# Performance work log

Hardware: AMD Instinct MI355X
Metric: run time of the kernel (lower is better)

Reference implementation:

```python
import jax, jax.numpy as jnp
import numpy as np

NUM_CODEBOOKS = 2
CODEBOOK_SIZE = 256
OUT_GROUP = 1
IN_GROUP = 8
IN_FEATURES = 4096
OUT_FEATURES = 11008


def setup_inputs() -> dict:
    key = jax.random.key(0)
    k1, k2, k3, k4, k5 = jax.random.split(key, 5)
    num_out_groups = OUT_FEATURES // OUT_GROUP
    num_in_groups = IN_FEATURES // IN_GROUP
    x = jax.random.normal(k1, (4, 2048, IN_FEATURES), dtype=jnp.float32)
    codes = jax.random.randint(k2, (num_out_groups, num_in_groups, NUM_CODEBOOKS), 0, CODEBOOK_SIZE, dtype=jnp.int32)
    codebooks = jax.random.normal(k3, (NUM_CODEBOOKS, CODEBOOK_SIZE, OUT_GROUP, IN_GROUP), dtype=jnp.float32) * 0.05
    scales = jax.random.uniform(k4, (num_out_groups, 1, 1, 1), dtype=jnp.float32)
    bias = jax.random.normal(k5, (OUT_FEATURES,), dtype=jnp.float32)
    return {"x": x, "codes": codes, "codebooks": codebooks, "scales": scales, "bias": bias}


def _dequantize_weight(codes, codebooks, scales):
    # codes: [Og, Ig, C] int; codebooks: [C, K, og, ig]; scales: [Og,1,1,1]
    C = codebooks.shape[0]
    og, ig = codebooks.shape[2], codebooks.shape[3]
    Og, Ig = codes.shape[0], codes.shape[1]
    # gather per-codebook vectors: result [Og, Ig, C, og, ig]
    w = codebooks[jnp.arange(C)[None, None, :], codes]
    w = w.sum(axis=2)                      # [Og, Ig, og, ig] (additive quantization)
    w = w * scales                         # broadcast [Og,1,1,1]
    w = w.transpose(0, 2, 1, 3)            # [Og, og, Ig, ig]
    return w.reshape(Og * og, Ig * ig)     # [out_features, in_features]


def reference(x, codes, codebooks, scales, bias):
    W = _dequantize_weight(codes, codebooks, scales)
    return jnp.einsum('bsi,oi->bso', x, W) + bias
```

## Files before the change

### kernel.cpp

```cpp
#include <hip/hip_runtime.h>
#include <hip/hip_bf16.h>
#include <stdint.h>

#define IN_F 4096
#define OUT_F 11008
#define M_ROWS 8192
#define NIG 512
#define CBSZ 256

typedef _Float16 f16x8 __attribute__((ext_vector_type(8)));
typedef float f32x4 __attribute__((ext_vector_type(4)));

__global__ __launch_bounds__(256) void dequant_w_kernel(
    const int* __restrict__ codes, const float* __restrict__ cbs,
    _Float16* __restrict__ W)
{
  const int idx = blockIdx.x * 256 + threadIdx.x;
  const int2 c = ((const int2*)codes)[idx];
  const float4* e0 = (const float4*)(cbs + (size_t)c.x * 8);
  const float4* e1 = (const float4*)(cbs + (size_t)CBSZ * 8 + (size_t)c.y * 8);
  const float4 a0 = e0[0], a1 = e0[1];
  const float4 b0 = e1[0], b1 = e1[1];
  f16x8 w;
  w[0] = (_Float16)(a0.x + b0.x);
  w[1] = (_Float16)(a0.y + b0.y);
  w[2] = (_Float16)(a0.z + b0.z);
  w[3] = (_Float16)(a0.w + b0.w);
  w[4] = (_Float16)(a1.x + b1.x);
  w[5] = (_Float16)(a1.y + b1.y);
  w[6] = (_Float16)(a1.z + b1.z);
  w[7] = (_Float16)(a1.w + b1.w);
  *(f16x8*)(W + (size_t)idx * 8) = w;
}

__global__ __launch_bounds__(256) void convert_x_kernel(
    const float* __restrict__ x, _Float16* __restrict__ X)
{
  const size_t i = ((size_t)blockIdx.x * 256 + threadIdx.x) * 8;
  const float4 a = *(const float4*)(x + i);
  const float4 b = *(const float4*)(x + i + 4);
  f16x8 v;
  v[0] = (_Float16)a.x; v[1] = (_Float16)a.y;
  v[2] = (_Float16)a.z; v[3] = (_Float16)a.w;
  v[4] = (_Float16)b.x; v[5] = (_Float16)b.y;
  v[6] = (_Float16)b.z; v[7] = (_Float16)b.w;
  *(f16x8*)(X + i) = v;
}

#define BM 256
#define BN 256
#define BK 64
#define NKT (IN_F / BK)
#define GRID_MT (M_ROWS / BM)
#define GRID_NT (OUT_F / BN)

__global__ __launch_bounds__(512, 2) void gemm_pipe(
    const _Float16* __restrict__ X, const _Float16* __restrict__ Wd,
    const float* __restrict__ scales, const float* __restrict__ bias,
    float* __restrict__ out)
{
  __shared__ char smem[131072];

  const int cpx = (GRID_MT * GRID_NT) >> 3;
  const int wg = (blockIdx.x & 7) * cpx + (blockIdx.x >> 3);
  const int mt = wg & (GRID_MT - 1), nt = wg >> 5;
  const int m0 = mt * BM, n0 = nt * BN;

  const int t_ = threadIdx.x;
  const int wave = t_ >> 6, lane = t_ & 63;
  const int wm = wave >> 2, wn = wave & 3;
  const int r16 = lane & 15;
  const int q = lane >> 4;
  const int sw = r16 & 7;
  const int c0 = ((q ^ sw) << 4);
  const int c1 = (((4 | q) ^ sw) << 4);

  const int s_row0 = t_ >> 3;
  const int s_col  = (((t_ & 7) ^ ((t_ >> 3) & 7)) << 3);
  const _Float16* asrc = X  + (size_t)(m0 + s_row0) * IN_F + s_col;
  const _Float16* bsrc = Wd + (size_t)(n0 + s_row0) * IN_F + s_col;
  const int s_dst = wave * 1024;

  f32x4 acc[8][4] = {};
  f16x8 al0[4], al1[4], ah0[4], ah1[4], bl0[2], bl1[2], bh0[2], bh1[2];

#define GLD(gsrc, ldst) __builtin_amdgcn_global_load_lds(                     \
    (const __attribute__((address_space(1))) void*)(gsrc),                    \
    (__attribute__((address_space(3))) void*)(ldst), 16, 0, 0)
#define STAGE_A(kt, bufc, i) GLD(asrc + (size_t)(kt) * BK + (size_t)(i) * 64 * IN_F, \
    smem + (bufc) * 65536 + (i) * 8192 + s_dst)
#define STAGE_B(kt, bufc, i) GLD(bsrc + (size_t)(kt) * BK + (size_t)(i) * 64 * IN_F, \
    smem + (bufc) * 65536 + 32768 + (i) * 8192 + s_dst)

#define RD_A(bufp, mm, cc) (*(const f16x8*)((bufp) + ((wm * 128 + (mm) * 16 + r16) << 7) + (cc)))
#define RD_B(bufp, nn, cc) (*(const f16x8*)((bufp) + 32768 + ((wn * 64 + (nn) * 16 + r16) << 7) + (cc)))

#define BAR   __builtin_amdgcn_s_barrier()
#define PRIO1 __builtin_amdgcn_s_setprio(1)
#define PRIO0 __builtin_amdgcn_s_setprio(0)
#define SBAR0 __builtin_amdgcn_sched_barrier(0)
#define VM0 asm volatile("s_waitcnt vmcnt(0)" ::: "memory")

#define MG(AF, BF, MO, NO)                                                    \
    _Pragma("unroll")                                                         \
    for (int m = 0; m < 4; ++m)                                               \
      _Pragma("unroll")                                                       \
      for (int n = 0; n < 2; ++n)                                             \
        acc[(MO) + m][(NO) + n] = __builtin_amdgcn_mfma_f32_16x16x32_f16(     \
            AF[m], BF[n], acc[(MO) + m][(NO) + n], 0, 0, 0)

#define TILE(P, tt, STG, GATE) do {                                           \
    const char* bufT = smem + (P) * 65536;                                    \
    if (STG) {                                                                \
      STAGE_A((tt) + 1, 1 - (P), 0); STAGE_A((tt) + 1, 1 - (P), 1);           \
      STAGE_A((tt) + 1, 1 - (P), 2); STAGE_A((tt) + 1, 1 - (P), 3);           \
      STAGE_B((tt) + 1, 1 - (P), 0); STAGE_B((tt) + 1, 1 - (P), 1);           \
      STAGE_B((tt) + 1, 1 - (P), 2); STAGE_B((tt) + 1, 1 - (P), 3);           \
    }                                                                         \
    SBAR0;                                                                    \
         \
    _Pragma("unroll")                                                         \
    for (int m = 0; m < 4; ++m) al0[m] = RD_A(bufT, m, c0);                   \
    _Pragma("unroll")                                                         \
    for (int n = 0; n < 2; ++n) { bl0[n] = RD_B(bufT, n, c0);                 \
                                  bh0[n] = RD_B(bufT, 2 + n, c0); }           \
    _Pragma("unroll")                                                         \
    for (int m = 0; m < 4; ++m) ah0[m] = RD_A(bufT, 4 + m, c0);               \
    SBAR0;                                                                    \
    PRIO1;                                                                    \
    MG(al0, bl0, 0, 0); MG(al0, bh0, 0, 2);                                   \
    MG(ah0, bh0, 4, 2); MG(ah0, bl0, 4, 0);                                   \
    PRIO0;                                                                    \
    SBAR0;                                                                    \
                                                           \
    _Pragma("unroll")                                                         \
    for (int m = 0; m < 4; ++m) al1[m] = RD_A(bufT, m, c1);                   \
    _Pragma("unroll")                                                         \
    for (int n = 0; n < 2; ++n) { bl1[n] = RD_B(bufT, n, c1);                 \
                                  bh1[n] = RD_B(bufT, 2 + n, c1); }           \
    _Pragma("unroll")                                                         \
    for (int m = 0; m < 4; ++m) ah1[m] = RD_A(bufT, 4 + m, c1);               \
    SBAR0;                                                                    \
    PRIO1;                                                                    \
    MG(al1, bl1, 0, 0); MG(al1, bh1, 0, 2);                                   \
    MG(ah1, bh1, 4, 2); MG(ah1, bl1, 4, 0);                                   \
    PRIO0;                                                                    \
    SBAR0;                                                                    \
    if (GATE) { VM0; BAR; }       \
  } while (0)

  STAGE_A(0, 0, 0); STAGE_A(0, 0, 1); STAGE_A(0, 0, 2); STAGE_A(0, 0, 3);
  STAGE_B(0, 0, 0); STAGE_B(0, 0, 1); STAGE_B(0, 0, 2); STAGE_B(0, 0, 3);
  VM0;
  BAR;

  #pragma unroll 1
  for (int t = 0; t < 62; t += 2) {
    TILE(0, t,     1, 1);
    TILE(1, t + 1, 1, 1);
  }
  TILE(0, 62, 1, 1);
  TILE(1, 63, 0, 0);

  const int crow = (lane >> 4) << 2;
  #pragma unroll
  for (int nf = 0; nf < 4; ++nf) {
    const int col = n0 + wn * 64 + nf * 16 + r16;
    const float s = scales[col];
    const float bb = bias[col];
    #pragma unroll
    for (int mf = 0; mf < 8; ++mf) {
      const int rb = m0 + wm * 128 + mf * 16 + crow;
      #pragma unroll
      for (int r = 0; r < 4; ++r)
        out[(size_t)(rb + r) * OUT_F + col] = acc[mf][nf][r] * s + bb;
    }
  }
#undef TILE
#undef MG
#undef RD_A
#undef RD_B
#undef STAGE_A
#undef STAGE_B
#undef GLD
}

__global__ __launch_bounds__(256) void naive_kernel(
    const float* __restrict__ x, const int* __restrict__ codes,
    const float* __restrict__ cbs, const float* __restrict__ scales,
    const float* __restrict__ bias, float* __restrict__ out)
{
  __shared__ float xrow[IN_F];
  const int m = blockIdx.x;
  for (int i = threadIdx.x; i < IN_F; i += 256)
    xrow[i] = x[(size_t)m * IN_F + i];
  __syncthreads();
  for (int o = threadIdx.x; o < OUT_F; o += 256) {
    float acc = 0.f;
    const int2* crow = (const int2*)codes + (size_t)o * NIG;
    for (int g = 0; g < NIG; ++g) {
      const int2 c = crow[g];
      const float* e0 = cbs + (size_t)c.x * 8;
      const float* e1 = cbs + (size_t)CBSZ * 8 + (size_t)c.y * 8;
      const float* xr = xrow + g * 8;
      #pragma unroll
      for (int j = 0; j < 8; ++j) acc += (e0[j] + e1[j]) * xr[j];
    }
    out[(size_t)m * OUT_F + o] = acc * scales[o] + bias[o];
  }
}

extern "C" void kernel_launch(void* const* d_in, const int* in_sizes, int n_in,
                              void* d_out, int out_size, void* d_ws, size_t ws_size,
                              hipStream_t stream) {
  const float* x      = (const float*)d_in[0];
  const int*   codes  = (const int*)d_in[1];
  const float* cbs    = (const float*)d_in[2];
  const float* scales = (const float*)d_in[3];
  const float* bias   = (const float*)d_in[4];
  float* out = (float*)d_out;

  const size_t W_BYTES = (size_t)OUT_F * IN_F * sizeof(_Float16);
  const size_t X_BYTES = (size_t)M_ROWS * IN_F * sizeof(_Float16);

  if (ws_size < W_BYTES + X_BYTES) {
    naive_kernel<<<M_ROWS, 256, 0, stream>>>(x, codes, cbs, scales, bias, out);
    return;
  }

  _Float16* W = (_Float16*)d_ws;
  _Float16* X = (_Float16*)((char*)d_ws + W_BYTES);

  dequant_w_kernel<<<(OUT_F * NIG) / 256, 256, 0, stream>>>(codes, cbs, W);
  convert_x_kernel<<<(M_ROWS * IN_F / 8) / 256, 256, 0, stream>>>(x, X);
  gemm_pipe<<<GRID_MT * GRID_NT, 512, 0, stream>>>(X, W, scales, bias, out);
}
```

Baseline: 854.8 us.

## Shrink GEMM tile to 128x128 with four waves and simpler schedule

Replaces the 256x256, 512-thread GEMM tile with a 128x128 tile run by 256 threads, halving shared memory to 64KB and the register accumulator to a 4x4 fragment grid. The hand-scheduled split of fragment loads and MFMA groups with sched barriers is dropped in favour of plain load-then-MFMA phases ending in __syncthreads. The intent is more workgroups and better occupancy or tail balance, at the cost of lower data reuse per tile and more global/L2 traffic for X and W. It also gives up the explicit vmcnt wait on the LDS-direct loads and relies on __syncthreads for ordering.

```diff
diff --git a/kernel.cpp b/kernel.cpp
--- a/kernel.cpp
+++ b/kernel.cpp
@@ -47,28 +47,28 @@
   *(f16x8*)(X + i) = v;
 }
 
-#define BM 256
-#define BN 256
+#define BM 128
+#define BN 128
 #define BK 64
 #define NKT (IN_F / BK)
 #define GRID_MT (M_ROWS / BM)
 #define GRID_NT (OUT_F / BN)
 
-__global__ __launch_bounds__(512, 2) void gemm_pipe(
+__global__ __launch_bounds__(256, 2) void gemm_128(
     const _Float16* __restrict__ X, const _Float16* __restrict__ Wd,
     const float* __restrict__ scales, const float* __restrict__ bias,
     float* __restrict__ out)
 {
-  __shared__ char smem[131072];
+  __shared__ char smem[65536];
 
   const int cpx = (GRID_MT * GRID_NT) >> 3;
   const int wg = (blockIdx.x & 7) * cpx + (blockIdx.x >> 3);
-  const int mt = wg & (GRID_MT - 1), nt = wg >> 5;
+  const int mt = wg & (GRID_MT - 1), nt = wg >> 6;
   const int m0 = mt * BM, n0 = nt * BN;
 
   const int t_ = threadIdx.x;
   const int wave = t_ >> 6, lane = t_ & 63;
-  const int wm = wave >> 2, wn = wave & 3;
+  const int wm = wave >> 1, wn = wave & 1;
   const int r16 = lane & 15;
   const int q = lane >> 4;
   const int sw = r16 & 7;
@@ -81,78 +81,57 @@
   const _Float16* bsrc = Wd + (size_t)(n0 + s_row0) * IN_F + s_col;
   const int s_dst = wave * 1024;
 
-  f32x4 acc[8][4] = {};
-  f16x8 al0[4], al1[4], ah0[4], ah1[4], bl0[2], bl1[2], bh0[2], bh1[2];
+  f32x4 acc[4][4] = {};
+  f16x8 af[4], bf[4];
 
 #define GLD(gsrc, ldst) __builtin_amdgcn_global_load_lds(                     \
     (const __attribute__((address_space(1))) void*)(gsrc),                    \
     (__attribute__((address_space(3))) void*)(ldst), 16, 0, 0)
-#define STAGE_A(kt, bufc, i) GLD(asrc + (size_t)(kt) * BK + (size_t)(i) * 64 * IN_F, \
-    smem + (bufc) * 65536 + (i) * 8192 + s_dst)
-#define STAGE_B(kt, bufc, i) GLD(bsrc + (size_t)(kt) * BK + (size_t)(i) * 64 * IN_F, \
-    smem + (bufc) * 65536 + 32768 + (i) * 8192 + s_dst)
-
-#define RD_A(bufp, mm, cc) (*(const f16x8*)((bufp) + ((wm * 128 + (mm) * 16 + r16) << 7) + (cc)))
-#define RD_B(bufp, nn, cc) (*(const f16x8*)((bufp) + 32768 + ((wn * 64 + (nn) * 16 + r16) << 7) + (cc)))
-
-#define BAR   __builtin_amdgcn_s_barrier()
+#define STAGE_A(kt, bufc, i) GLD(asrc + (size_t)(kt) * BK + (size_t)(i) * 32 * IN_F, \
+    smem + (bufc) * 32768 + (i) * 4096 + s_dst)
+#define STAGE_B(kt, bufc, i) GLD(bsrc + (size_t)(kt) * BK + (size_t)(i) * 32 * IN_F, \
+    smem + (bufc) * 32768 + 16384 + (i) * 4096 + s_dst)
+
+#define RD_A(bufp, mf, cc) (*(const f16x8*)((bufp) + ((wm * 64 + (mf) * 16 + r16) << 7) + (cc)))
+#define RD_B(bufp, nf, cc) (*(const f16x8*)((bufp) + 16384 + ((wn * 64 + (nf) * 16 + r16) << 7) + (cc)))
+
 #define PRIO1 __builtin_amdgcn_s_setprio(1)
 #define PRIO0 __builtin_amdgcn_s_setprio(0)
-#define SBAR0 __builtin_amdgcn_sched_barrier(0)
-#define VM0 asm volatile("s_waitcnt vmcnt(0)" ::: "memory")
-
-#define MG(AF, BF, MO, NO)                                                    \
-    _Pragma("unroll")                                                         \
-    for (int m = 0; m < 4; ++m)                                               \
+
+#define MG                                                                    \
+    _Pragma("unroll")                                                         \
+    for (int mf = 0; mf < 4; ++mf)                                            \
       _Pragma("unroll")                                                       \
-      for (int n = 0; n < 2; ++n)                                             \
-        acc[(MO) + m][(NO) + n] = __builtin_amdgcn_mfma_f32_16x16x32_f16(     \
-            AF[m], BF[n], acc[(MO) + m][(NO) + n], 0, 0, 0)
-
-#define TILE(P, tt, STG, GATE) do {                                           \
-    const char* bufT = smem + (P) * 65536;                                    \
+      for (int nf = 0; nf < 4; ++nf)                                          \
+        acc[mf][nf] = __builtin_amdgcn_mfma_f32_16x16x32_f16(                 \
+            af[mf], bf[nf], acc[mf][nf], 0, 0, 0)
+
+#define TILE(P, tt, STG, SYNC) do {                                           \
+    const char* bufT = smem + (P) * 32768;                                    \
     if (STG) {                                                                \
       STAGE_A((tt) + 1, 1 - (P), 0); STAGE_A((tt) + 1, 1 - (P), 1);           \
       STAGE_A((tt) + 1, 1 - (P), 2); STAGE_A((tt) + 1, 1 - (P), 3);           \
       STAGE_B((tt) + 1, 1 - (P), 0); STAGE_B((tt) + 1, 1 - (P), 1);           \
       STAGE_B((tt) + 1, 1 - (P), 2); STAGE_B((tt) + 1, 1 - (P), 3);           \
     }                                                                         \
-    SBAR0;                                                                    \
-         \
-    _Pragma("unroll")                                                         \
-    for (int m = 0; m < 4; ++m) al0[m] = RD_A(bufT, m, c0);                   \
-    _Pragma("unroll")                                                         \
-    for (int n = 0; n < 2; ++n) { bl0[n] = RD_B(bufT, n, c0);                 \
-                                  bh0[n] = RD_B(bufT, 2 + n, c0); }           \
-    _Pragma("unroll")                                                         \
-    for (int m = 0; m < 4; ++m) ah0[m] = RD_A(bufT, 4 + m, c0);               \
-    SBAR0;                                                                    \
-    PRIO1;                                                                    \
-    MG(al0, bl0, 0, 0); MG(al0, bh0, 0, 2);                                   \
-    MG(ah0, bh0, 4, 2); MG(ah0, bl0, 4, 0);                                   \
-    PRIO0;                                                                    \
-    SBAR0;                                                                    \
-                                                           \
-    _Pragma("unroll")                                                         \
-    for (int m = 0; m < 4; ++m) al1[m] = RD_A(bufT, m, c1);                   \
-    _Pragma("unroll")                                                         \
-    for (int n = 0; n < 2; ++n) { bl1[n] = RD_B(bufT, n, c1);                 \
-                                  bh1[n] = RD_B(bufT, 2 + n, c1); }           \
-    _Pragma("unroll")                                                         \
-    for (int m = 0; m < 4; ++m) ah1[m] = RD_A(bufT, 4 + m, c1);               \
-    SBAR0;                                                                    \
-    PRIO1;                                                                    \
-    MG(al1, bl1, 0, 0); MG(al1, bh1, 0, 2);                                   \
-    MG(ah1, bh1, 4, 2); MG(ah1, bl1, 4, 0);                                   \
-    PRIO0;                                                                    \
-    SBAR0;                                                                    \
-    if (GATE) { VM0; BAR; }       \
+              \
+    _Pragma("unroll")                                                         \
+    for (int mf = 0; mf < 4; ++mf) af[mf] = RD_A(bufT, mf, c0);               \
+    _Pragma("unroll")                                                         \
+    for (int nf = 0; nf < 4; ++nf) bf[nf] = RD_B(bufT, nf, c0);               \
+    PRIO1; MG; PRIO0;                                                         \
+                                                                \
+    _Pragma("unroll")                                                         \
+    for (int mf = 0; mf < 4; ++mf) af[mf] = RD_A(bufT, mf, c1);               \
+    _Pragma("unroll")                                                         \
+    for (int nf = 0; nf < 4; ++nf) bf[nf] = RD_B(bufT, nf, c1);               \
+    PRIO1; MG; PRIO0;                                                         \
+    if (SYNC) __syncthreads();   \
   } while (0)
 
   STAGE_A(0, 0, 0); STAGE_A(0, 0, 1); STAGE_A(0, 0, 2); STAGE_A(0, 0, 3);
   STAGE_B(0, 0, 0); STAGE_B(0, 0, 1); STAGE_B(0, 0, 2); STAGE_B(0, 0, 3);
-  VM0;
-  BAR;
+  __syncthreads();
 
   #pragma unroll 1
   for (int t = 0; t < 62; t += 2) {
@@ -169,8 +148,8 @@
     const float s = scales[col];
     const float bb = bias[col];
     #pragma unroll
-    for (int mf = 0; mf < 8; ++mf) {
-      const int rb = m0 + wm * 128 + mf * 16 + crow;
+    for (int mf = 0; mf < 4; ++mf) {
+      const int rb = m0 + wm * 64 + mf * 16 + crow;
       #pragma unroll
       for (int r = 0; r < 4; ++r)
         out[(size_t)(rb + r) * OUT_F + col] = acc[mf][nf][r] * s + bb;
@@ -233,5 +212,5 @@
 
   dequant_w_kernel<<<(OUT_F * NIG) / 256, 256, 0, stream>>>(codes, cbs, W);
   convert_x_kernel<<<(M_ROWS * IN_F / 8) / 256, 256, 0, stream>>>(x, X);
-  gemm_pipe<<<GRID_MT * GRID_NT, 512, 0, stream>>>(X, W, scales, bias, out);
-}
+  gemm_128<<<GRID_MT * GRID_NT, 256, 0, stream>>>(X, W, scales, bias, out);
+}
```

Result: slower. 1.016 ms (+18.9%).
